# Performance work log

Hardware: AMD Instinct MI355X
Metric: run time of the kernel (lower is better)

The kernel has to match this reference:

```python
import jax, jax.numpy as jnp
import numpy as np

B, TQ, TK = 2, 2048, 2048
D, H, G = 1024, 16, 4
HD = D // H  # 64
MAX_LEN = 4096


def _rope(x, max_len):
    # x: [B, H, S, hd]; interleaved even/odd RoPE, freqs use full head_dim in denom
    hd = x.shape[-1]
    seq = x.shape[2]
    pos = jnp.arange(max_len, dtype=jnp.float32)[:, None]           # [max_len, 1]
    div = jnp.exp(jnp.arange(0, hd, 2, dtype=jnp.float32) * (-np.log(10000.0) / hd))
    sin = jnp.sin(pos * div)[:seq]                                   # [S, hd/2]
    cos = jnp.cos(pos * div)[:seq]
    xe, xo = x[..., 0::2], x[..., 1::2]
    oe = xe * cos - xo * sin
    oo = xe * sin + xo * cos
    return jnp.stack([oe, oo], axis=-1).reshape(x.shape)


def setup_inputs() -> dict:
    key = jax.random.key(0)
    ks = jax.random.split(key, 10)
    s = 0.02
    return {
        "X": jax.random.normal(ks[0], (B, TQ, D), jnp.float32),
        "encoder_output": jax.random.normal(ks[1], (B, TK, D), jnp.float32),
        "Wq": jax.random.normal(ks[2], (D, D), jnp.float32) * s,
        "bq": jnp.zeros((D,), jnp.float32),
        "Wk": jax.random.normal(ks[3], (D, G * HD), jnp.float32) * s,
        "bk": jnp.zeros((G * HD,), jnp.float32),
        "Wv": jax.random.normal(ks[4], (D, G * HD), jnp.float32) * s,
        "bv": jnp.zeros((G * HD,), jnp.float32),
        "Wo": jax.random.normal(ks[5], (D, D), jnp.float32) * s,
        "bo": jnp.zeros((D,), jnp.float32),
        "max_len": MAX_LEN,
    }


def reference(X, encoder_output, Wq, bq, Wk, bk, Wv, bv, Wo, bo, max_len):
    bsz, tq, d = X.shape
    q = X @ Wq + bq                       # [B, TQ, D]
    k = encoder_output @ Wk + bk          # [B, TK, G*HD]
    v = encoder_output @ Wv + bv

    q = q.reshape(bsz, tq, H, HD).transpose(0, 2, 1, 3)          # [B, H, TQ, HD]
    k = k.reshape(bsz, -1, G, HD).transpose(0, 2, 1, 3)          # [B, G, TK, HD]
    v = v.reshape(bsz, -1, G, HD).transpose(0, 2, 1, 3)
    # expand each group to H//G consecutive heads (matches torch expand+reshape)
    k = jnp.repeat(k, H // G, axis=1)                            # [B, H, TK, HD]
    v = jnp.repeat(v, H // G, axis=1)

    q = _rope(q, max_len)
    k = _rope(k, max_len)

    scores = jnp.einsum("bhqd,bhkd->bhqk", q, k) / jnp.sqrt(jnp.float32(HD))
    w = jax.nn.softmax(scores, axis=-1)
    o = jnp.einsum("bhqk,bhkd->bhqd", w, v)                      # [B, H, TQ, HD]
    o = o.transpose(0, 2, 1, 3).reshape(bsz, tq, d)
    return o @ Wo + bo
```

## Files before the change

kernel.cpp:

```cpp
#include <hip/hip_runtime.h>
#include <cstdint>


typedef __bf16 bf16x8 __attribute__((ext_vector_type(8)));
typedef __bf16 bf16x4v __attribute__((ext_vector_type(4)));
typedef float f32x4 __attribute__((ext_vector_type(4)));

#define MFMA16(a, b, c) __builtin_amdgcn_mfma_f32_16x16x32_bf16((a), (b), (c), 0, 0, 0)

constexpr int Bc = 2, TQc = 2048, TKc = 2048, Dc = 1024, Hc = 16, Gc = 4, HDc = 64;
constexpr float QSCALE = 0.18033688011112042f;

__device__ __forceinline__ ushort bfbits(float x) {
  __bf16 h = (__bf16)x;
  return __builtin_bit_cast(ushort, h);
}

__device__ __forceinline__ float fexp2(float x) {
  float r;
  asm("v_exp_f32 %0, %1" : "=v"(r) : "v"(x));
  return r;
}

__device__ __forceinline__ float fmax3(float a, float b, float c) {
  return fmaxf(fmaxf(a, b), c);
}

__device__ __forceinline__ void async_lds16(void* lds, const void* g) {
  __builtin_amdgcn_global_load_lds((const __attribute__((address_space(1))) uint32_t*)g,
                                   (__attribute__((address_space(3))) uint32_t*)lds,
                                   16, 0, 0);
}

__global__ __launch_bounds__(256) void prep_k(const float* __restrict__ X,
                                              const float* __restrict__ E,
                                              const float* __restrict__ Wq,
                                              const float* __restrict__ Wo,
                                              const float* __restrict__ Wk,
                                              const float* __restrict__ Wv,
                                              ushort* __restrict__ Xb,
                                              ushort* __restrict__ Eb,
                                              ushort* __restrict__ Wqt,
                                              ushort* __restrict__ Wot,
                                              ushort* __restrict__ Wkvt) {
  __shared__ float t[64][65];
  const int bid = blockIdx.x;
  if (bid < 8192) {
    const float* s = (bid < 4096) ? X : E;
    ushort* d = (bid < 4096) ? Xb : Eb;
    int i = (bid & 4095) * 256 + threadIdx.x;
    float4 v = reinterpret_cast<const float4*>(s)[i];
    ushort4 o;
    o.x = bfbits(v.x); o.y = bfbits(v.y); o.z = bfbits(v.z); o.w = bfbits(v.w);
    reinterpret_cast<ushort4*>(d)[i] = o;
    return;
  }
  const int w = bid - 8192;
  const int z = w >> 8, rem = w & 255;
  const int bx = rem & 15, by = rem >> 4;
  const float* src;
  ushort* dst;
  int C, c0;
  if (z == 0)      { src = Wq; dst = Wqt; C = 1024; c0 = bx * 64; }
  else if (z == 1) { src = Wo; dst = Wot; C = 1024; c0 = bx * 64; }
  else {
    if (bx >= 8) return;
    if (bx < 4) { src = Wk; dst = Wkvt; }
    else        { src = Wv; dst = Wkvt + 256 * 1024; }
    C = 256; c0 = (bx & 3) * 64;
  }
  const int r0 = by * 64;
  const int tx = threadIdx.x & 63, ty = threadIdx.x >> 6;
#pragma unroll
  for (int i = 0; i < 16; ++i) {
    int r = i * 4 + ty;
    t[r][tx] = src[(size_t)(r0 + r) * C + c0 + tx];
  }
  __syncthreads();
#pragma unroll
  for (int i = 0; i < 16; ++i) {
    int c = i * 4 + ty;
    dst[(size_t)(c0 + c) * 1024 + r0 + tx] = bfbits(t[tx][c]);
  }
}

__device__ __forceinline__ void gemm_mainloop(const ushort* __restrict__ A,
                                              const ushort* __restrict__ Bt,
                                              int m0, int n0, int K,
                                              char* sA, char* sB,
                                              f32x4 acc[4][2]) {
  const int lane = threadIdx.x & 63, wid = threadIdx.x >> 6;
  const int l15 = lane & 15, l4 = lane >> 4;
  const int wr = (wid >> 1) * 64, wc = (wid & 1) * 32;
  const int srow = lane >> 3;
  const int scc = (lane & 7) ^ (srow & 7);
  const int rxr = l15 & 7;

  const int nsteps = K >> 6;
#pragma unroll
  for (int j = 0; j < 4; ++j) {
    int c = wid * 4 + j;
    async_lds16(sA + c * 1024, A + (size_t)(m0 + c * 8 + srow) * K + scc * 8);
  }
#pragma unroll
  for (int j = 0; j < 2; ++j) {
    int c = wid * 2 + j;
    async_lds16(sB + c * 1024, Bt + (size_t)(n0 + c * 8 + srow) * K + scc * 8);
  }
  __syncthreads();

  int buf = 0;
  for (int s2 = 0; s2 < nsteps; ++s2) {
    if (s2 + 1 < nsteps) {
      const int k0 = (s2 + 1) * 64;
      char* dA = sA + (buf ^ 1) * 16384;
      char* dB = sB + (buf ^ 1) * 8192;
#pragma unroll
      for (int j = 0; j < 4; ++j) {
        int c = wid * 4 + j;
        async_lds16(dA + c * 1024, A + (size_t)(m0 + c * 8 + srow) * K + k0 + scc * 8);
      }
#pragma unroll
      for (int j = 0; j < 2; ++j) {
        int c = wid * 2 + j;
        async_lds16(dB + c * 1024, Bt + (size_t)(n0 + c * 8 + srow) * K + k0 + scc * 8);
      }
    }
    const char* aB = sA + buf * 16384;
    const char* bB = sB + buf * 8192;
    bf16x8 af[2][4], bfr[2][2];
#pragma unroll
    for (int mi = 0; mi < 4; ++mi) {
      const int row = wr + mi * 16 + l15;
#pragma unroll
      for (int kk = 0; kk < 2; ++kk)
        af[kk][mi] = *reinterpret_cast<const bf16x8*>(
            aB + row * 128 + (((l4 + kk * 4) ^ rxr) << 4));
    }
#pragma unroll
    for (int ni = 0; ni < 2; ++ni) {
      const int row = wc + ni * 16 + l15;
#pragma unroll
      for (int kk = 0; kk < 2; ++kk)
        bfr[kk][ni] = *reinterpret_cast<const bf16x8*>(
            bB + row * 128 + (((l4 + kk * 4) ^ rxr) << 4));
    }
#pragma unroll
    for (int kk = 0; kk < 2; ++kk)
#pragma unroll
      for (int mi = 0; mi < 4; ++mi)
#pragma unroll
        for (int ni = 0; ni < 2; ++ni)
          acc[mi][ni] = MFMA16(af[kk][mi], bfr[kk][ni], acc[mi][ni]);
    __syncthreads();
    buf ^= 1;
  }
}

__device__ __forceinline__ void gemm_epilogue(f32x4 acc[4][2], int mode, int m0,
                                              int n0, const float* b0,
                                              const float* b1, float* Cf,
                                              ushort* U0, ushort* U1, int N) {
  const int lane = threadIdx.x & 63, wid = threadIdx.x >> 6;
  const int l15 = lane & 15, l4 = lane >> 4;
  const int wr = (wid >> 1) * 64, wc = (wid & 1) * 32;
#pragma unroll
  for (int ni = 0; ni < 2; ++ni) {
    const int col = n0 + wc + ni * 16 + l15;
    if (mode == 0) {
      const float bv = b0[col];
#pragma unroll
      for (int mi = 0; mi < 4; ++mi) {
        const int rowb = m0 + wr + mi * 16 + l4 * 4;
#pragma unroll
        for (int r = 0; r < 4; ++r)
          Cf[(size_t)(rowb + r) * N + col] = acc[mi][ni][r] + bv;
      }
    } else if (mode == 1) {
      const int h = col >> 6, d = col & 63, fi = d >> 1, odd = d & 1;
      const float div = __expf(-0.28782313662425572f * (float)fi);
      const float bv = b0[col];
#pragma unroll
      for (int mi = 0; mi < 4; ++mi) {
        const int rowb = m0 + wr + mi * 16 + l4 * 4;
#pragma unroll
        for (int r = 0; r < 4; ++r) {
          const int row = rowb + r, b = row >> 11, t = row & 2047;
          const float val = acc[mi][ni][r] + bv;
          const float prt = __shfl_xor(val, 1);
          float sn, cs;
          __sincosf((float)t * div, &sn, &cs);
          const float o = odd ? (prt * sn + val * cs) : (val * cs - prt * sn);
          U0[(((size_t)(b * Hc + h)) * TQc + t) * HDc + d] = bfbits(o * QSCALE);
        }
      }
    } else {
      if (col < 256) {
        const int g = col >> 6, d = col & 63, fi = d >> 1, odd = d & 1;
        const float div = __expf(-0.28782313662425572f * (float)fi);
        const float bv = b0[col];
#pragma unroll
        for (int mi = 0; mi < 4; ++mi) {
          const int rowb = m0 + wr + mi * 16 + l4 * 4;
#pragma unroll
          for (int r = 0; r < 4; ++r) {
            const int row = rowb + r, b = row >> 11, t = row & 2047;
            const float val = acc[mi][ni][r] + bv;
            const float prt = __shfl_xor(val, 1);
            float sn, cs;
            __sincosf((float)t * div, &sn, &cs);
            const float o = odd ? (prt * sn + val * cs) : (val * cs - prt * sn);
            U0[(((size_t)(b * Gc + g)) * TKc + t) * HDc + d] = bfbits(o);
          }
        }
      } else {
        const int c2 = col - 256;
        const int g = c2 >> 6, d = c2 & 63;
        const float bv = b1[c2];
#pragma unroll
        for (int mi = 0; mi < 4; ++mi) {
          const int rowb = m0 + wr + mi * 16 + l4 * 4;
          const int b = rowb >> 11, t0 = rowb & 2047;
          ushort4 w;
          w.x = bfbits(acc[mi][ni][0] + bv);
          w.y = bfbits(acc[mi][ni][1] + bv);
          w.z = bfbits(acc[mi][ni][2] + bv);
          w.w = bfbits(acc[mi][ni][3] + bv);
          *reinterpret_cast<ushort4*>(
              &U1[(((size_t)(b * Gc + g)) * HDc + d) * TKc + t0]) = w;
        }
      }
    }
  }
}

__global__ __launch_bounds__(256) void qkv_k(const ushort* __restrict__ Xb,
                                             const ushort* __restrict__ Eb,
                                             const ushort* __restrict__ Wqt,
                                             const ushort* __restrict__ Wkvt,
                                             const float* __restrict__ bq,
                                             const float* __restrict__ bk,
                                             const float* __restrict__ bv,
                                             ushort* __restrict__ Qb,
                                             ushort* __restrict__ Kb,
                                             ushort* __restrict__ Vt) {
  __shared__ __attribute__((aligned(16))) char smem[48 * 1024];
  const int bid = blockIdx.x;
  const ushort *A, *Bt;
  const float *b0, *b1 = nullptr;
  ushort *U0, *U1 = nullptr;
  int mode, tb, tn;
  if (bid < 512) { A = Xb; Bt = Wqt; b0 = bq; U0 = Qb; mode = 1; tb = bid; tn = 16; }
  else { A = Eb; Bt = Wkvt; b0 = bk; b1 = bv; U0 = Kb; U1 = Vt; mode = 2; tb = bid - 512; tn = 8; }
  const int m0 = (tb / tn) * 128, n0 = (tb % tn) * 64;
  const f32x4 z = {0.f, 0.f, 0.f, 0.f};
  f32x4 acc[4][2] = {{z, z}, {z, z}, {z, z}, {z, z}};
  gemm_mainloop(A, Bt, m0, n0, 1024, smem, smem + 32768, acc);
  gemm_epilogue(acc, mode, m0, n0, b0, b1, nullptr, U0, U1, 0);
}

__global__ __launch_bounds__(256) void oproj_k(const ushort* __restrict__ Ob,
                                               const ushort* __restrict__ Wot,
                                               const float* __restrict__ bo,
                                               float* __restrict__ out) {
  __shared__ __attribute__((aligned(16))) char smem[48 * 1024];
  const int bid = blockIdx.x;
  const int m0 = (bid >> 4) * 128, n0 = (bid & 15) * 64;
  const f32x4 z = {0.f, 0.f, 0.f, 0.f};
  f32x4 acc[4][2] = {{z, z}, {z, z}, {z, z}, {z, z}};
  gemm_mainloop(Ob, Wot, m0, n0, 1024, smem, smem + 32768, acc);
  gemm_epilogue(acc, 0, m0, n0, bo, nullptr, out, nullptr, nullptr, 1024);
}

__global__ __launch_bounds__(512, 4) void attn_k(const ushort* __restrict__ Qg,
                                                 const ushort* __restrict__ Kg,
                                                 const ushort* __restrict__ Vg,
                                                 ushort* __restrict__ Ob) {
  __shared__ __attribute__((aligned(16))) char smem[48 * 1024];
  const int lane = threadIdx.x & 63, wid = threadIdx.x >> 6;
  const int l15 = lane & 15, l4 = lane >> 4;
  const int bid = blockIdx.x;
  const int bg = bid & 7, pos = bid >> 3;
  const int b = bg >> 2, g = bg & 3;
  const int h = g * 4 + (pos >> 4);
  const int q0 = (pos & 15) * 128 + wid * 16;
  const ushort* Qp = Qg + ((size_t)(b * Hc + h)) * TQc * HDc;
  const ushort* Kp = Kg + ((size_t)(b * Gc + g)) * TKc * HDc;
  const ushort* Vp = Vg + ((size_t)(b * Gc + g)) * HDc * TKc;
  char* sK = smem;
  char* sV = smem + 16384;
  char* pb = smem + 32768 + wid * 2048;
  const int rx = (l15 & 7) << 4;
  const int swz = l15 & 7;

  const int sr = wid * 8 + (lane >> 3);
  const int sc = (lane & 7) ^ ((lane >> 3) & 7);
  const char* Kb8 = (const char*)Kp;
  const char* Vb8 = (const char*)Vp;

  bf16x8 bq0 = *reinterpret_cast<const bf16x8*>(Qp + (size_t)(q0 + l15) * HDc + l4 * 8);
  bf16x8 bq1 = *reinterpret_cast<const bf16x8*>(Qp + (size_t)(q0 + l15) * HDc + 32 + l4 * 8);

  float m = -INFINITY, l = 0.f;
  const f32x4 z = {0.f, 0.f, 0.f, 0.f};
  f32x4 accO[4] = {z, z, z, z};

  constexpr int NT = TKc / 64;
  async_lds16(sK + wid * 1024, Kb8 + (size_t)sr * 128 + sc * 16);
  async_lds16(sV + wid * 1024, Vb8 + (size_t)sr * (TKc * 2) + sc * 16);
  __syncthreads();

  int buf = 0;
  for (int kt = 0; kt < NT; ++kt) {
    if (kt + 1 < NT) {
      char* dK = sK + (buf ^ 1) * 8192 + wid * 1024;
      char* dV = sV + (buf ^ 1) * 8192 + wid * 1024;
      async_lds16(dK, Kb8 + ((size_t)(kt + 1) * 64 + sr) * 128 + sc * 16);
      async_lds16(dV, Vb8 + (size_t)sr * (TKc * 2) + (size_t)(kt + 1) * 128 + sc * 16);
    }
    const char* sKb = sK + buf * 8192;
    const char* sVb = sV + buf * 8192;

    f32x4 s[4] = {z, z, z, z};
#pragma unroll
    for (int nf = 0; nf < 4; ++nf) {
      const char* krow = sKb + (nf * 16 + l15) * 128;
      bf16x8 k0 = *reinterpret_cast<const bf16x8*>(krow + ((l4 ^ swz) << 4));
      bf16x8 k1 = *reinterpret_cast<const bf16x8*>(krow + (((4 + l4) ^ swz) << 4));
      s[nf] = MFMA16(k0, bq0, s[nf]);
      s[nf] = MFMA16(k1, bq1, s[nf]);
    }
    bf16x8 va[4][2];
#pragma unroll
    for (int df = 0; df < 4; ++df) {
      const char* vrow = sVb + (df * 16 + l15) * 128;
      va[df][0] = *reinterpret_cast<const bf16x8*>(vrow + ((l4 ^ swz) << 4));
      va[df][1] = *reinterpret_cast<const bf16x8*>(vrow + (((4 + l4) ^ swz) << 4));
    }

    float pm = fmax3(fmax3(s[0][0], s[0][1], s[0][2]),
                     fmax3(s[0][3], s[1][0], s[1][1]),
                     fmax3(s[1][2], s[1][3], s[2][0]));
    pm = fmax3(pm,
               fmax3(s[2][1], s[2][2], s[2][3]),
               fmax3(s[3][0], s[3][1], fmaxf(s[3][2], s[3][3])));
    pm = fmaxf(pm, __shfl_xor(pm, 16));
    pm = fmaxf(pm, __shfl_xor(pm, 32));
    if (!__all(pm - m <= 11.5f)) {
      float mn = fmaxf(m, pm);
      float sc2 = fexp2(m - mn);
      m = mn;
      l *= sc2;
#pragma unroll
      for (int df = 0; df < 4; ++df) accO[df] *= sc2;
    }
    float ps = 0.f;
#pragma unroll
    for (int nf = 0; nf < 4; ++nf)
#pragma unroll
      for (int r = 0; r < 4; ++r) {
        float p = fexp2(s[nf][r] - m);
        s[nf][r] = p;
        ps += p;
      }
    ps += __shfl_xor(ps, 16);
    ps += __shfl_xor(ps, 32);
    l += ps;

#pragma unroll
    for (int nf = 0; nf < 4; ++nf) {
      bf16x4v pv;
      pv[0] = (__bf16)s[nf][0];
      pv[1] = (__bf16)s[nf][1];
      pv[2] = (__bf16)s[nf][2];
      pv[3] = (__bf16)s[nf][3];
      *reinterpret_cast<uint2*>(pb + l15 * 128 + ((nf * 32 + l4 * 8) ^ rx)) =
          __builtin_bit_cast(uint2, pv);
    }
    asm volatile("" ::: "memory");
    bf16x8 ap0 = *reinterpret_cast<const bf16x8*>(pb + l15 * 128 + ((l4 * 16) ^ rx));
    bf16x8 ap1 = *reinterpret_cast<const bf16x8*>(pb + l15 * 128 + ((64 + l4 * 16) ^ rx));
#pragma unroll
    for (int df = 0; df < 4; ++df)
      accO[df] = MFMA16(ap1, va[df][1], MFMA16(ap0, va[df][0], accO[df]));

    __syncthreads();
    buf ^= 1;
  }

  float inv[4];
#pragma unroll
  for (int r = 0; r < 4; ++r) inv[r] = 1.f / __shfl(l, l4 * 4 + r);
#pragma unroll
  for (int df = 0; df < 4; ++df)
#pragma unroll
    for (int r = 0; r < 4; ++r) {
      int row = q0 + l4 * 4 + r;
      int col = h * HDc + df * 16 + l15;
      Ob[((size_t)b * TQc + row) * Dc + col] = bfbits(accO[df][r] * inv[r]);
    }
}

extern "C" void kernel_launch(void* const* d_in, const int* in_sizes, int n_in,
                              void* d_out, int out_size, void* d_ws, size_t ws_size,
                              hipStream_t stream) {
  const float* X  = (const float*)d_in[0];
  const float* E  = (const float*)d_in[1];
  const float* Wq = (const float*)d_in[2];
  const float* bq = (const float*)d_in[3];
  const float* Wk = (const float*)d_in[4];
  const float* bk = (const float*)d_in[5];
  const float* Wv = (const float*)d_in[6];
  const float* bv = (const float*)d_in[7];
  const float* Wo = (const float*)d_in[8];
  const float* bo = (const float*)d_in[9];
  float* out = (float*)d_out;
  char* ws = (char*)d_ws;

  const size_t MB = 1ull << 20;
  if (ws_size < 42 * MB) return;

  ushort* Xb   = (ushort*)(ws + 0 * MB);
  ushort* Eb   = (ushort*)(ws + 8 * MB);
  ushort* Wqt  = (ushort*)(ws + 16 * MB);
  ushort* Wkvt = (ushort*)(ws + 18 * MB);
  ushort* Wot  = (ushort*)(ws + 19 * MB);
  ushort* Qb   = (ushort*)(ws + 21 * MB);
  ushort* Kb   = (ushort*)(ws + 29 * MB);
  ushort* Vt   = (ushort*)(ws + 31 * MB);
  ushort* Ob   = (ushort*)(ws + 33 * MB);

  prep_k<<<dim3(8960), 256, 0, stream>>>(X, E, Wq, Wo, Wk, Wv, Xb, Eb, Wqt, Wot, Wkvt);
  qkv_k<<<dim3(768), 256, 0, stream>>>(Xb, Eb, Wqt, Wkvt, bq, bk, bv, Qb, Kb, Vt);
  attn_k<<<dim3(512), dim3(512), 0, stream>>>(Qb, Kb, Vt, Ob);
  oproj_k<<<dim3(512), 256, 0, stream>>>(Ob, Wot, bo, out);
}
```

Baseline: 105.2 us.

## Triple-buffer K/V tiles in attention with explicit vmcnt waits and one barrier

Switches the attention kernel's K/V staging from double to triple buffering, with a prefetch distance of two tiles. Explicit s_waitcnt vmcnt waits plus a single barrier at the top of each iteration replace the end-of-loop __syncthreads. The goal is to hide global-to-LDS latency better and to drop one barrier per iteration. The cost is more LDS (64KB vs 48KB), which with 512-thread blocks and launch_bounds(512,4) may cut the number of resident blocks per CU.

```diff
diff --git a/kernel.cpp b/kernel.cpp
--- a/kernel.cpp
+++ b/kernel.cpp
@@ -276,7 +276,7 @@
                                                  const ushort* __restrict__ Kg,
                                                  const ushort* __restrict__ Vg,
                                                  ushort* __restrict__ Ob) {
-  __shared__ __attribute__((aligned(16))) char smem[48 * 1024];
+  __shared__ __attribute__((aligned(16))) char smem[64 * 1024];
   const int lane = threadIdx.x & 63, wid = threadIdx.x >> 6;
   const int l15 = lane & 15, l4 = lane >> 4;
   const int bid = blockIdx.x;
@@ -287,16 +287,20 @@
   const ushort* Qp = Qg + ((size_t)(b * Hc + h)) * TQc * HDc;
   const ushort* Kp = Kg + ((size_t)(b * Gc + g)) * TKc * HDc;
   const ushort* Vp = Vg + ((size_t)(b * Gc + g)) * HDc * TKc;
-  char* sK = smem;
-  char* sV = smem + 16384;
-  char* pb = smem + 32768 + wid * 2048;
+  char* k0 = smem;
+  char* k1 = smem + 8192;
+  char* k2 = smem + 16384;
+  char* v0 = smem + 24576;
+  char* v1 = smem + 32768;
+  char* v2 = smem + 40960;
+  char* pb = smem + 49152 + wid * 2048;
   const int rx = (l15 & 7) << 4;
   const int swz = l15 & 7;
 
   const int sr = wid * 8 + (lane >> 3);
   const int sc = (lane & 7) ^ ((lane >> 3) & 7);
-  const char* Kb8 = (const char*)Kp;
-  const char* Vb8 = (const char*)Vp;
+  const char* KstN = (const char*)Kp + (size_t)sr * 128 + sc * 16;
+  const char* VstN = (const char*)Vp + (size_t)sr * (TKc * 2) + sc * 16;
 
   bf16x8 bq0 = *reinterpret_cast<const bf16x8*>(Qp + (size_t)(q0 + l15) * HDc + l4 * 8);
   bf16x8 bq1 = *reinterpret_cast<const bf16x8*>(Qp + (size_t)(q0 + l15) * HDc + 32 + l4 * 8);
@@ -306,34 +310,37 @@
   f32x4 accO[4] = {z, z, z, z};
 
   constexpr int NT = TKc / 64;
-  async_lds16(sK + wid * 1024, Kb8 + (size_t)sr * 128 + sc * 16);
-  async_lds16(sV + wid * 1024, Vb8 + (size_t)sr * (TKc * 2) + sc * 16);
-  __syncthreads();
-
-  int buf = 0;
+  async_lds16(k0 + wid * 1024, KstN);
+  async_lds16(v0 + wid * 1024, VstN);
+  KstN += 8192; VstN += 128;
+  async_lds16(k1 + wid * 1024, KstN);
+  async_lds16(v1 + wid * 1024, VstN);
+  KstN += 8192; VstN += 128;
+
   for (int kt = 0; kt < NT; ++kt) {
-    if (kt + 1 < NT) {
-      char* dK = sK + (buf ^ 1) * 8192 + wid * 1024;
-      char* dV = sV + (buf ^ 1) * 8192 + wid * 1024;
-      async_lds16(dK, Kb8 + ((size_t)(kt + 1) * 64 + sr) * 128 + sc * 16);
-      async_lds16(dV, Vb8 + (size_t)sr * (TKc * 2) + (size_t)(kt + 1) * 128 + sc * 16);
-    }
-    const char* sKb = sK + buf * 8192;
-    const char* sVb = sV + buf * 8192;
+    if (kt < NT - 1) asm volatile("s_waitcnt vmcnt(2)" ::: "memory");
+    else             asm volatile("s_waitcnt vmcnt(0)" ::: "memory");
+    __builtin_amdgcn_s_barrier();
+    __builtin_amdgcn_sched_barrier(0);
+    if (kt + 2 < NT) {
+      async_lds16(k2 + wid * 1024, KstN);
+      async_lds16(v2 + wid * 1024, VstN);
+      KstN += 8192; VstN += 128;
+    }
 
     f32x4 s[4] = {z, z, z, z};
 #pragma unroll
     for (int nf = 0; nf < 4; ++nf) {
-      const char* krow = sKb + (nf * 16 + l15) * 128;
-      bf16x8 k0 = *reinterpret_cast<const bf16x8*>(krow + ((l4 ^ swz) << 4));
-      bf16x8 k1 = *reinterpret_cast<const bf16x8*>(krow + (((4 + l4) ^ swz) << 4));
-      s[nf] = MFMA16(k0, bq0, s[nf]);
-      s[nf] = MFMA16(k1, bq1, s[nf]);
+      const char* krow = k0 + (nf * 16 + l15) * 128;
+      bf16x8 kf0 = *reinterpret_cast<const bf16x8*>(krow + ((l4 ^ swz) << 4));
+      bf16x8 kf1 = *reinterpret_cast<const bf16x8*>(krow + (((4 + l4) ^ swz) << 4));
+      s[nf] = MFMA16(kf0, bq0, s[nf]);
+      s[nf] = MFMA16(kf1, bq1, s[nf]);
     }
     bf16x8 va[4][2];
 #pragma unroll
     for (int df = 0; df < 4; ++df) {
-      const char* vrow = sVb + (df * 16 + l15) * 128;
+      const char* vrow = v0 + (df * 16 + l15) * 128;
       va[df][0] = *reinterpret_cast<const bf16x8*>(vrow + ((l4 ^ swz) << 4));
       va[df][1] = *reinterpret_cast<const bf16x8*>(vrow + (((4 + l4) ^ swz) << 4));
     }
@@ -384,8 +391,8 @@
     for (int df = 0; df < 4; ++df)
       accO[df] = MFMA16(ap1, va[df][1], MFMA16(ap0, va[df][0], accO[df]));
 
-    __syncthreads();
-    buf ^= 1;
+    char* tk = k0; k0 = k1; k1 = k2; k2 = tk;
+    char* tv = v0; v0 = v1; v1 = v2; v2 = tv;
   }
 
   float inv[4];
```

Result: no change. 105.5 us (+0.3%).
